# Performance work log

Hardware: AMD Instinct MI355X
Metric: run time of the kernel (lower is better)

The kernel has to match this reference:

```python
import jax, jax.numpy as jnp
import numpy as np

TAU = 0.07
EPS = 1e-6  # torch CosineSimilarity eps


def setup_inputs() -> dict:
    key = jax.random.key(0)
    k1, k2, k3 = jax.random.split(key, 3)
    n, d, n_classes = 8192, 256, 1024
    imitation_embeds = jax.random.normal(k1, (n, d), dtype=jnp.float32)
    recording_embeds = jax.random.normal(k2, (n, d), dtype=jnp.float32)
    labels = jax.random.randint(k3, (n,), 0, n_classes, dtype=jnp.int64)
    return {
        "imitation_embeds": imitation_embeds,
        "recording_embeds": recording_embeds,
        "labels": labels,
    }


def reference(imitation_embeds, recording_embeds, labels):
    n = imitation_embeds.shape[0]
    # cosine similarity with per-vector norm clamp (torch semantics)
    im_n = imitation_embeds / jnp.maximum(
        jnp.linalg.norm(imitation_embeds, axis=1, keepdims=True), EPS)
    rec_n = recording_embeds / jnp.maximum(
        jnp.linalg.norm(recording_embeds, axis=1, keepdims=True), EPS)
    i2r = jnp.einsum("nd,md->nm", im_n, rec_n) / TAU  # [n, n]

    same = labels[:, None] == labels[None, :]          # [n, n] bool
    eye = jnp.eye(n, dtype=bool)
    # original: mask = ~(same ^ diag_embed(diag(same))); diag(same) is all True
    # -> keep the diagonal (positive) and all different-label negatives
    mask = ~(same ^ eye)

    # per-row masked log-softmax evaluated at the diagonal entry:
    # log_softmax(row[mask])[pos_of_diag] = i2r[i,i] - logsumexp(row over mask)
    lse = jax.nn.logsumexp(jnp.where(mask, i2r, -jnp.inf), axis=1)  # [n]
    loss = -jnp.mean(jnp.diagonal(i2r) - lse)
    return loss
```

## Files before the change

kernel.cpp:

```cpp
#include <hip/hip_runtime.h>

#define N 8192
#define D 256
#define INV_TAU 14.285714285714286f
#define SCALE2 20.60992915555662f
#define EPSN 1e-6f
#define MAXM 48

#define RT 256
#define CT 64
#define CSPLIT 16
#define CPB (N / CSPLIT)
#define NTILES (CPB / CT)

typedef unsigned int u32x4 __attribute__((ext_vector_type(4)));
typedef __bf16 bf16x8 __attribute__((ext_vector_type(8)));
typedef float f32x4 __attribute__((ext_vector_type(4)));

__device__ inline unsigned short f2bf(float x) {
    unsigned int u = __builtin_bit_cast(unsigned int, x);
    u += 0x7fffu + ((u >> 16) & 1u);
    return (unsigned short)(u >> 16);
}
__device__ inline float b2f(unsigned short u) {
    unsigned int x = (unsigned int)u << 16;
    return __builtin_bit_cast(float, x);
}
__device__ inline float fexp2(float x) {
#if __has_builtin(__builtin_amdgcn_exp2f)
    return __builtin_amdgcn_exp2f(x);
#else
    return __expf(x * 0.6931471805599453f);
#endif
}

__global__ void ntx_prep(const float* __restrict__ im, const float* __restrict__ rec,
                         const int* __restrict__ labels,
                         unsigned short* __restrict__ A, unsigned short* __restrict__ Bm,
                         float* __restrict__ diag, float* __restrict__ rowsum,
                         int* __restrict__ cnt, unsigned short* __restrict__ members) {
    const int wave = threadIdx.x >> 6;
    const int lane = threadIdx.x & 63;
    const int row  = blockIdx.x * 4 + wave;

    const float4 a = ((const float4*)(im  + (size_t)row * D))[lane];
    const float4 b = ((const float4*)(rec + (size_t)row * D))[lane];

    float ssa = a.x*a.x + a.y*a.y + a.z*a.z + a.w*a.w;
    float ssb = b.x*b.x + b.y*b.y + b.z*b.z + b.w*b.w;
    float dt  = a.x*b.x + a.y*b.y + a.z*b.z + a.w*b.w;
    #pragma unroll
    for (int o = 32; o; o >>= 1) {
        ssa += __shfl_xor(ssa, o);
        ssb += __shfl_xor(ssb, o);
        dt  += __shfl_xor(dt , o);
    }
    const float ra = 1.0f / fmaxf(sqrtf(ssa), EPSN);
    const float rb = 1.0f / fmaxf(sqrtf(ssb), EPSN);

    ushort4 pa, pb;
    pa.x = f2bf(a.x*ra); pa.y = f2bf(a.y*ra); pa.z = f2bf(a.z*ra); pa.w = f2bf(a.w*ra);
    pb.x = f2bf(b.x*rb); pb.y = f2bf(b.y*rb); pb.z = f2bf(b.z*rb); pb.w = f2bf(b.w*rb);

    *(ushort4*)(A + (size_t)row * D + lane * 4) = pa;
    const int chunk = lane >> 1;
    const int sw = chunk ^ (row & 7);
    *(ushort4*)(Bm + (size_t)row * D + sw * 8 + (lane & 1) * 4) = pb;

    if (lane == 0) {
        diag[row]   = dt * ra * rb * INV_TAU;
        rowsum[row] = 0.0f;
        const int lab = labels[row];
        const int u = atomicAdd(&cnt[lab], 1);
        if (u < MAXM) members[lab * MAXM + u] = (unsigned short)row;
    }
}

__global__ __launch_bounds__(256, 2)
void ntx_lse(const unsigned short* __restrict__ A, const unsigned short* __restrict__ Bm,
             float* __restrict__ rowsum) {
    __shared__ __align__(16) unsigned short Bs[CT][D];

    const int wave = threadIdx.x >> 6;
    const int lane = threadIdx.x & 63;
    const int g    = lane >> 4;
    const int n16  = lane & 15;

    const int rowblk = blockIdx.x & (N / RT - 1);
    const int colblk = blockIdx.x >> 5;
    const int row0 = rowblk * RT + wave * 64;
    const int col0 = colblk * CPB;

    bf16x8 afrag[4][8];
    #pragma unroll
    for (int rs = 0; rs < 4; ++rs) {
        const int r = row0 + rs * 16 + n16;
        #pragma unroll
        for (int k = 0; k < 8; ++k)
            afrag[rs][k] = __builtin_bit_cast(
                bf16x8, *(const u32x4*)(A + (size_t)r * D + k * 32 + g * 8));
    }

    float acc[4][4];
    #pragma unroll
    for (int rs = 0; rs < 4; ++rs)
        #pragma unroll
        for (int q = 0; q < 4; ++q) acc[rs][q] = 0.f;

    for (int t = 0; t < NTILES; ++t) {
        const char* gsrc = (const char*)(Bm + (size_t)(col0 + t * CT) * D);
        char* lbase = (char*)&Bs[0][0];
        #pragma unroll
        for (int i = 0; i < 8; ++i) {
            const int off = (i * 4 + wave) * 1024;
            __builtin_amdgcn_global_load_lds(
                (const __attribute__((address_space(1))) void*)(gsrc + off + lane * 16),
                (__attribute__((address_space(3))) void*)(lbase + off),
                16, 0, 0);
        }
        __syncthreads();

        #pragma unroll
        for (int cs = 0; cs < 4; ++cs) {
            const int bc = cs * 16 + n16;
            bf16x8 bfrag[8];
            #pragma unroll
            for (int k = 0; k < 8; ++k)
                bfrag[k] = __builtin_bit_cast(
                    bf16x8, *(const u32x4*)(&Bs[bc][((k * 4 + g) ^ (bc & 7)) * 8]));

            #pragma unroll
            for (int rs = 0; rs < 4; ++rs) {
                f32x4 c = {0.f, 0.f, 0.f, 0.f};
                #pragma unroll
                for (int k = 0; k < 8; ++k)
                    c = __builtin_amdgcn_mfma_f32_16x16x32_bf16(
                            afrag[rs][k], bfrag[k], c, 0, 0, 0);
                #pragma unroll
                for (int q = 0; q < 4; ++q)
                    acc[rs][q] += fexp2(c[q] * SCALE2);
            }
        }
        __syncthreads();
    }

    #pragma unroll
    for (int rs = 0; rs < 4; ++rs)
        #pragma unroll
        for (int q = 0; q < 4; ++q) {
            float v = acc[rs][q];
            v += __shfl_xor(v, 1);
            v += __shfl_xor(v, 2);
            v += __shfl_xor(v, 4);
            v += __shfl_xor(v, 8);
            if (n16 == 0)
                atomicAdd(&rowsum[row0 + rs * 16 + g * 4 + q], v);
        }
}

__global__ void ntx_correct(const unsigned short* __restrict__ A,
                            const unsigned short* __restrict__ Bm,
                            const int* __restrict__ labels, const int* __restrict__ cnt,
                            const unsigned short* __restrict__ members,
                            float* __restrict__ rowsum) {
    const int wave = threadIdx.x >> 6;
    const int lane = threadIdx.x & 63;
    const int W = blockIdx.x * 4 + wave;
    const int chunk = lane >> 1;

    for (int rr = 0; rr < 4; ++rr) {
        const int r = W * 4 + rr;
        const int lab = labels[r];
        const int m = min(cnt[lab], MAXM);
        const ushort4 av = *(const ushort4*)(A + (size_t)r * D + lane * 4);
        const float a0 = b2f(av.x), a1 = b2f(av.y), a2 = b2f(av.z), a3 = b2f(av.w);
        float sum = 0.f;
        for (int t = 0; t < m; ++t) {
            const int j = members[lab * MAXM + t];
            if (j == r) continue;
            const int sw = chunk ^ (j & 7);
            const ushort4 bv = *(const ushort4*)(Bm + (size_t)j * D + sw * 8 + (lane & 1) * 4);
            float d = a0 * b2f(bv.x) + a1 * b2f(bv.y) + a2 * b2f(bv.z) + a3 * b2f(bv.w);
            #pragma unroll
            for (int o = 32; o; o >>= 1) d += __shfl_xor(d, o);
            sum += fexp2(d * SCALE2);
        }
        if (lane == 0) rowsum[r] -= sum;
    }
}

__global__ void ntx_finish(const float* __restrict__ diag,
                           const float* __restrict__ rowsum,
                           float* __restrict__ out) {
    __shared__ float red[256];
    float s = 0.f;
    for (int i = threadIdx.x; i < N; i += 256)
        s += logf(rowsum[i]) - diag[i];
    red[threadIdx.x] = s;
    __syncthreads();
    #pragma unroll
    for (int o = 128; o; o >>= 1) {
        if (threadIdx.x < o) red[threadIdx.x] += red[threadIdx.x + o];
        __syncthreads();
    }
    if (threadIdx.x == 0) out[0] = red[0] / (float)N;
}

extern "C" void kernel_launch(void* const* d_in, const int* in_sizes, int n_in,
                              void* d_out, int out_size, void* d_ws, size_t ws_size,
                              hipStream_t stream) {
    const float* im     = (const float*)d_in[0];
    const float* rec    = (const float*)d_in[1];
    const int*   labels = (const int*)d_in[2];
    float* out = (float*)d_out;

    unsigned short* A  = (unsigned short*)d_ws;
    unsigned short* Bm = A + (size_t)N * D;
    float* diag   = (float*)(Bm + (size_t)N * D);
    float* rowsum = diag + N;
    int* cnt      = (int*)(rowsum + N);
    unsigned short* members = (unsigned short*)(cnt + 1024);

    hipMemsetAsync(cnt, 0, 1024 * sizeof(int), stream);
    ntx_prep<<<N / 4, 256, 0, stream>>>(im, rec, labels, A, Bm, diag, rowsum, cnt, members);
    ntx_lse<<<(N / RT) * CSPLIT, 256, 0, stream>>>(A, Bm, rowsum);
    ntx_correct<<<N / 16, 256, 0, stream>>>(A, Bm, labels, cnt, members, rowsum);
    ntx_finish<<<1, 256, 0, stream>>>(diag, rowsum, out);
}
```

Baseline: 149.7 us.

## Double-buffer LDS tiles, fold exp scale into A, move log into correction kernel

The LSE kernel now double-buffers the B tile in LDS, prefetching the next tile before computing the current one and dropping one barrier per iteration. The SCALE2 factor is folded into the normalized A rows during prep, which removes a multiply per exponent in the inner loop. The correction kernel now uses one wave per row and computes the per-row log term, so the final reduction only sums precomputed values. The changes cost double the LDS footprint, which may affect occupancy, and add rounding risk because the scaled bf16 values are not unit vectors.

```diff
diff --git a/kernel.cpp b/kernel.cpp
--- a/kernel.cpp
+++ b/kernel.cpp
@@ -4,8 +4,9 @@
 #define D 256
 #define INV_TAU 14.285714285714286f
 #define SCALE2 20.60992915555662f
+#define LN2F 0.6931471805599453f
 #define EPSN 1e-6f
-#define MAXM 48
+#define MAXM 64
 
 #define RT 256
 #define CT 64
@@ -55,8 +56,8 @@
         ssb += __shfl_xor(ssb, o);
         dt  += __shfl_xor(dt , o);
     }
-    const float ra = 1.0f / fmaxf(sqrtf(ssa), EPSN);
-    const float rb = 1.0f / fmaxf(sqrtf(ssb), EPSN);
+    const float ra = SCALE2 / fmaxf(sqrtf(ssa), EPSN);
+    const float rb = 1.0f   / fmaxf(sqrtf(ssb), EPSN);
 
     ushort4 pa, pb;
     pa.x = f2bf(a.x*ra); pa.y = f2bf(a.y*ra); pa.z = f2bf(a.z*ra); pa.w = f2bf(a.w*ra);
@@ -68,7 +69,7 @@
     *(ushort4*)(Bm + (size_t)row * D + sw * 8 + (lane & 1) * 4) = pb;
 
     if (lane == 0) {
-        diag[row]   = dt * ra * rb * INV_TAU;
+        diag[row]   = (dt / SCALE2) * ra * rb * INV_TAU;
         rowsum[row] = 0.0f;
         const int lab = labels[row];
         const int u = atomicAdd(&cnt[lab], 1);
@@ -79,7 +80,7 @@
 __global__ __launch_bounds__(256, 2)
 void ntx_lse(const unsigned short* __restrict__ A, const unsigned short* __restrict__ Bm,
              float* __restrict__ rowsum) {
-    __shared__ __align__(16) unsigned short Bs[CT][D];
+    __shared__ __align__(16) unsigned short Bs[2][CT][D];
 
     const int wave = threadIdx.x >> 6;
     const int lane = threadIdx.x & 63;
@@ -107,18 +108,28 @@
         #pragma unroll
         for (int q = 0; q < 4; ++q) acc[rs][q] = 0.f;
 
+    const char* gbase = (const char*)(Bm + (size_t)col0 * D);
+
+    #define STAGE(t, buf)                                                          \
+        {                                                                          \
+            const char* gsrc = gbase + (t) * (CT * D * 2);                         \
+            char* lbase = (char*)&Bs[buf][0][0];                                   \
+            _Pragma("unroll")                                                      \
+            for (int i = 0; i < 8; ++i) {                                          \
+                const int off = (i * 4 + wave) * 1024;                             \
+                __builtin_amdgcn_global_load_lds(                                  \
+                    (const __attribute__((address_space(1))) void*)(gsrc + off + lane * 16), \
+                    (__attribute__((address_space(3))) void*)(lbase + off),        \
+                    16, 0, 0);                                                     \
+            }                                                                      \
+        }
+
+    STAGE(0, 0)
+
     for (int t = 0; t < NTILES; ++t) {
-        const char* gsrc = (const char*)(Bm + (size_t)(col0 + t * CT) * D);
-        char* lbase = (char*)&Bs[0][0];
-        #pragma unroll
-        for (int i = 0; i < 8; ++i) {
-            const int off = (i * 4 + wave) * 1024;
-            __builtin_amdgcn_global_load_lds(
-                (const __attribute__((address_space(1))) void*)(gsrc + off + lane * 16),
-                (__attribute__((address_space(3))) void*)(lbase + off),
-                16, 0, 0);
-        }
         __syncthreads();
+        if (t + 1 < NTILES) STAGE(t + 1, (t + 1) & 1)
+        const int buf = t & 1;
 
         #pragma unroll
         for (int cs = 0; cs < 4; ++cs) {
@@ -127,7 +138,7 @@
             #pragma unroll
             for (int k = 0; k < 8; ++k)
                 bfrag[k] = __builtin_bit_cast(
-                    bf16x8, *(const u32x4*)(&Bs[bc][((k * 4 + g) ^ (bc & 7)) * 8]));
+                    bf16x8, *(const u32x4*)(&Bs[buf][bc][((k * 4 + g) ^ (bc & 7)) * 8]));
 
             #pragma unroll
             for (int rs = 0; rs < 4; ++rs) {
@@ -138,10 +149,9 @@
                             afrag[rs][k], bfrag[k], c, 0, 0, 0);
                 #pragma unroll
                 for (int q = 0; q < 4; ++q)
-                    acc[rs][q] += fexp2(c[q] * SCALE2);
+                    acc[rs][q] += fexp2(c[q]);
             }
         }
-        __syncthreads();
     }
 
     #pragma unroll
@@ -158,44 +168,43 @@
         }
 }
 
-__global__ void ntx_correct(const unsigned short* __restrict__ A,
-                            const unsigned short* __restrict__ Bm,
-                            const int* __restrict__ labels, const int* __restrict__ cnt,
-                            const unsigned short* __restrict__ members,
-                            float* __restrict__ rowsum) {
+__global__ void ntx_corr(const unsigned short* __restrict__ A,
+                         const unsigned short* __restrict__ Bm,
+                         const int* __restrict__ labels, const int* __restrict__ cnt,
+                         const unsigned short* __restrict__ members,
+                         const float* __restrict__ diag,
+                         const float* __restrict__ rowsum,
+                         float* __restrict__ loss) {
     const int wave = threadIdx.x >> 6;
     const int lane = threadIdx.x & 63;
-    const int W = blockIdx.x * 4 + wave;
+    const int r = blockIdx.x * 4 + wave;
     const int chunk = lane >> 1;
 
-    for (int rr = 0; rr < 4; ++rr) {
-        const int r = W * 4 + rr;
-        const int lab = labels[r];
-        const int m = min(cnt[lab], MAXM);
-        const ushort4 av = *(const ushort4*)(A + (size_t)r * D + lane * 4);
-        const float a0 = b2f(av.x), a1 = b2f(av.y), a2 = b2f(av.z), a3 = b2f(av.w);
-        float sum = 0.f;
-        for (int t = 0; t < m; ++t) {
-            const int j = members[lab * MAXM + t];
-            if (j == r) continue;
-            const int sw = chunk ^ (j & 7);
-            const ushort4 bv = *(const ushort4*)(Bm + (size_t)j * D + sw * 8 + (lane & 1) * 4);
-            float d = a0 * b2f(bv.x) + a1 * b2f(bv.y) + a2 * b2f(bv.z) + a3 * b2f(bv.w);
-            #pragma unroll
-            for (int o = 32; o; o >>= 1) d += __shfl_xor(d, o);
-            sum += fexp2(d * SCALE2);
-        }
-        if (lane == 0) rowsum[r] -= sum;
-    }
-}
-
-__global__ void ntx_finish(const float* __restrict__ diag,
-                           const float* __restrict__ rowsum,
-                           float* __restrict__ out) {
+    const int lab = labels[r];
+    const int m = min(cnt[lab], MAXM);
+
+    const ushort4 av = *(const ushort4*)(A + (size_t)r * D + lane * 4);
+    const float a0 = b2f(av.x), a1 = b2f(av.y), a2 = b2f(av.z), a3 = b2f(av.w);
+
+    float sum = 0.f;
+    for (int t = 0; t < m; ++t) {
+        const int j = members[lab * MAXM + t];
+        if (j == r) continue;
+        const int sw = chunk ^ (j & 7);
+        const ushort4 bv = *(const ushort4*)(Bm + (size_t)j * D + sw * 8 + (lane & 1) * 4);
+        float d = a0 * b2f(bv.x) + a1 * b2f(bv.y) + a2 * b2f(bv.z) + a3 * b2f(bv.w);
+        #pragma unroll
+        for (int o = 32; o; o >>= 1) d += __shfl_xor(d, o);
+        sum += fexp2(d);
+    }
+    if (lane == 0)
+        loss[r] = log2f(rowsum[r] - sum) * LN2F - diag[r];
+}
+
+__global__ void ntx_final(const float* __restrict__ loss, float* __restrict__ out) {
     __shared__ float red[256];
     float s = 0.f;
-    for (int i = threadIdx.x; i < N; i += 256)
-        s += logf(rowsum[i]) - diag[i];
+    for (int i = threadIdx.x; i < N; i += 256) s += loss[i];
     red[threadIdx.x] = s;
     __syncthreads();
     #pragma unroll
@@ -218,12 +227,13 @@
     unsigned short* Bm = A + (size_t)N * D;
     float* diag   = (float*)(Bm + (size_t)N * D);
     float* rowsum = diag + N;
-    int* cnt      = (int*)(rowsum + N);
+    float* loss   = rowsum + N;
+    int* cnt      = (int*)(loss + N);
     unsigned short* members = (unsigned short*)(cnt + 1024);
 
     hipMemsetAsync(cnt, 0, 1024 * sizeof(int), stream);
     ntx_prep<<<N / 4, 256, 0, stream>>>(im, rec, labels, A, Bm, diag, rowsum, cnt, members);
     ntx_lse<<<(N / RT) * CSPLIT, 256, 0, stream>>>(A, Bm, rowsum);
-    ntx_correct<<<N / 16, 256, 0, stream>>>(A, Bm, labels, cnt, members, rowsum);
-    ntx_finish<<<1, 256, 0, stream>>>(diag, rowsum, out);
-}
+    ntx_corr<<<N / 4, 256, 0, stream>>>(A, Bm, labels, cnt, members, diag, rowsum, loss);
+    ntx_final<<<1, 256, 0, stream>>>(loss, out);
+}
```

Result: faster. 127.8 us (-14.6%).

## Shrink LSE row tile, double column split, fold scale into A, fuse finish

Applied to the files above, without the earlier changes.

Halves the per-wave row tile in the LSE kernel and doubles the column split, raising launch-bounds occupancy to 4 blocks. Folds the exp2 scale factor into the normalized A rows so the inner loop skips a multiply. Merges the final reduction into the correction kernel with a per-block atomicAdd, removing one launch. The smaller tile halves B-fragment reuse per wave, adding LDS traffic per MFMA, and the scaling before bf16 rounding slightly changes numerics.

```diff
diff --git a/kernel.cpp b/kernel.cpp
--- a/kernel.cpp
+++ b/kernel.cpp
@@ -4,12 +4,13 @@
 #define D 256
 #define INV_TAU 14.285714285714286f
 #define SCALE2 20.60992915555662f
+#define LN2F 0.6931471805599453f
 #define EPSN 1e-6f
-#define MAXM 48
-
-#define RT 256
+#define MAXM 64
+
+#define RT 128
 #define CT 64
-#define CSPLIT 16
+#define CSPLIT 32
 #define CPB (N / CSPLIT)
 #define NTILES (CPB / CT)
 
@@ -38,7 +39,8 @@
                          const int* __restrict__ labels,
                          unsigned short* __restrict__ A, unsigned short* __restrict__ Bm,
                          float* __restrict__ diag, float* __restrict__ rowsum,
-                         int* __restrict__ cnt, unsigned short* __restrict__ members) {
+                         int* __restrict__ cnt, unsigned short* __restrict__ members,
+                         float* __restrict__ out) {
     const int wave = threadIdx.x >> 6;
     const int lane = threadIdx.x & 63;
     const int row  = blockIdx.x * 4 + wave;
@@ -55,8 +57,8 @@
         ssb += __shfl_xor(ssb, o);
         dt  += __shfl_xor(dt , o);
     }
-    const float ra = 1.0f / fmaxf(sqrtf(ssa), EPSN);
-    const float rb = 1.0f / fmaxf(sqrtf(ssb), EPSN);
+    const float ra = SCALE2 / fmaxf(sqrtf(ssa), EPSN);
+    const float rb = 1.0f   / fmaxf(sqrtf(ssb), EPSN);
 
     ushort4 pa, pb;
     pa.x = f2bf(a.x*ra); pa.y = f2bf(a.y*ra); pa.z = f2bf(a.z*ra); pa.w = f2bf(a.w*ra);
@@ -68,15 +70,16 @@
     *(ushort4*)(Bm + (size_t)row * D + sw * 8 + (lane & 1) * 4) = pb;
 
     if (lane == 0) {
-        diag[row]   = dt * ra * rb * INV_TAU;
+        diag[row]   = (dt / SCALE2) * ra * rb * INV_TAU;
         rowsum[row] = 0.0f;
         const int lab = labels[row];
         const int u = atomicAdd(&cnt[lab], 1);
         if (u < MAXM) members[lab * MAXM + u] = (unsigned short)row;
-    }
-}
-
-__global__ __launch_bounds__(256, 2)
+        if (row == 0) out[0] = 0.0f;
+    }
+}
+
+__global__ __launch_bounds__(256, 4)
 void ntx_lse(const unsigned short* __restrict__ A, const unsigned short* __restrict__ Bm,
              float* __restrict__ rowsum) {
     __shared__ __align__(16) unsigned short Bs[CT][D];
@@ -87,13 +90,13 @@
     const int n16  = lane & 15;
 
     const int rowblk = blockIdx.x & (N / RT - 1);
-    const int colblk = blockIdx.x >> 5;
-    const int row0 = rowblk * RT + wave * 64;
+    const int colblk = blockIdx.x >> 6;
+    const int row0 = rowblk * RT + wave * 32;
     const int col0 = colblk * CPB;
 
-    bf16x8 afrag[4][8];
+    bf16x8 afrag[2][8];
     #pragma unroll
-    for (int rs = 0; rs < 4; ++rs) {
+    for (int rs = 0; rs < 2; ++rs) {
         const int r = row0 + rs * 16 + n16;
         #pragma unroll
         for (int k = 0; k < 8; ++k)
@@ -101,22 +104,22 @@
                 bf16x8, *(const u32x4*)(A + (size_t)r * D + k * 32 + g * 8));
     }
 
-    float acc[4][4];
-    #pragma unroll
-    for (int rs = 0; rs < 4; ++rs)
-        #pragma unroll
-        for (int q = 0; q < 4; ++q) acc[rs][q] = 0.f;
+    float acc[2][4] = {{0.f,0.f,0.f,0.f},{0.f,0.f,0.f,0.f}};
+
+    const char* gbase = (const char*)(Bm + (size_t)col0 * D);
 
     for (int t = 0; t < NTILES; ++t) {
-        const char* gsrc = (const char*)(Bm + (size_t)(col0 + t * CT) * D);
-        char* lbase = (char*)&Bs[0][0];
-        #pragma unroll
-        for (int i = 0; i < 8; ++i) {
-            const int off = (i * 4 + wave) * 1024;
-            __builtin_amdgcn_global_load_lds(
-                (const __attribute__((address_space(1))) void*)(gsrc + off + lane * 16),
-                (__attribute__((address_space(3))) void*)(lbase + off),
-                16, 0, 0);
+        {
+            const char* gsrc = gbase + t * (CT * D * 2);
+            char* lbase = (char*)&Bs[0][0];
+            #pragma unroll
+            for (int i = 0; i < 8; ++i) {
+                const int off = (i * 4 + wave) * 1024;
+                __builtin_amdgcn_global_load_lds(
+                    (const __attribute__((address_space(1))) void*)(gsrc + off + lane * 16),
+                    (__attribute__((address_space(3))) void*)(lbase + off),
+                    16, 0, 0);
+            }
         }
         __syncthreads();
 
@@ -130,7 +133,7 @@
                     bf16x8, *(const u32x4*)(&Bs[bc][((k * 4 + g) ^ (bc & 7)) * 8]));
 
             #pragma unroll
-            for (int rs = 0; rs < 4; ++rs) {
+            for (int rs = 0; rs < 2; ++rs) {
                 f32x4 c = {0.f, 0.f, 0.f, 0.f};
                 #pragma unroll
                 for (int k = 0; k < 8; ++k)
@@ -138,14 +141,14 @@
                             afrag[rs][k], bfrag[k], c, 0, 0, 0);
                 #pragma unroll
                 for (int q = 0; q < 4; ++q)
-                    acc[rs][q] += fexp2(c[q] * SCALE2);
+                    acc[rs][q] += fexp2(c[q]);
             }
         }
         __syncthreads();
     }
 
     #pragma unroll
-    for (int rs = 0; rs < 4; ++rs)
+    for (int rs = 0; rs < 2; ++rs)
         #pragma unroll
         for (int q = 0; q < 4; ++q) {
             float v = acc[rs][q];
@@ -158,22 +161,28 @@
         }
 }
 
-__global__ void ntx_correct(const unsigned short* __restrict__ A,
-                            const unsigned short* __restrict__ Bm,
-                            const int* __restrict__ labels, const int* __restrict__ cnt,
-                            const unsigned short* __restrict__ members,
-                            float* __restrict__ rowsum) {
+__global__ void ntx_corr(const unsigned short* __restrict__ A,
+                         const unsigned short* __restrict__ Bm,
+                         const int* __restrict__ labels, const int* __restrict__ cnt,
+                         const unsigned short* __restrict__ members,
+                         const float* __restrict__ diag,
+                         const float* __restrict__ rowsum,
+                         float* __restrict__ out) {
+    __shared__ float wred[4];
     const int wave = threadIdx.x >> 6;
     const int lane = threadIdx.x & 63;
-    const int W = blockIdx.x * 4 + wave;
+    const int w = blockIdx.x * 4 + wave;
     const int chunk = lane >> 1;
 
+    float lsum = 0.f;
     for (int rr = 0; rr < 4; ++rr) {
-        const int r = W * 4 + rr;
+        const int r = w * 4 + rr;
         const int lab = labels[r];
         const int m = min(cnt[lab], MAXM);
+
         const ushort4 av = *(const ushort4*)(A + (size_t)r * D + lane * 4);
         const float a0 = b2f(av.x), a1 = b2f(av.y), a2 = b2f(av.z), a3 = b2f(av.w);
+
         float sum = 0.f;
         for (int t = 0; t < m; ++t) {
             const int j = members[lab * MAXM + t];
@@ -183,27 +192,14 @@
             float d = a0 * b2f(bv.x) + a1 * b2f(bv.y) + a2 * b2f(bv.z) + a3 * b2f(bv.w);
             #pragma unroll
             for (int o = 32; o; o >>= 1) d += __shfl_xor(d, o);
-            sum += fexp2(d * SCALE2);
-        }
-        if (lane == 0) rowsum[r] -= sum;
-    }
-}
-
-__global__ void ntx_finish(const float* __restrict__ diag,
-                           const float* __restrict__ rowsum,
-                           float* __restrict__ out) {
-    __shared__ float red[256];
-    float s = 0.f;
-    for (int i = threadIdx.x; i < N; i += 256)
-        s += logf(rowsum[i]) - diag[i];
-    red[threadIdx.x] = s;
+            sum += fexp2(d);
+        }
+        lsum += log2f(rowsum[r] - sum) * LN2F - diag[r];
+    }
+    if (lane == 0) wred[wave] = lsum;
     __syncthreads();
-    #pragma unroll
-    for (int o = 128; o; o >>= 1) {
-        if (threadIdx.x < o) red[threadIdx.x] += red[threadIdx.x + o];
-        __syncthreads();
-    }
-    if (threadIdx.x == 0) out[0] = red[0] / (float)N;
+    if (threadIdx.x == 0)
+        atomicAdd(out, (wred[0] + wred[1] + wred[2] + wred[3]) * (1.0f / (float)N));
 }
 
 extern "C" void kernel_launch(void* const* d_in, const int* in_sizes, int n_in,
@@ -222,8 +218,7 @@
     unsigned short* members = (unsigned short*)(cnt + 1024);
 
     hipMemsetAsync(cnt, 0, 1024 * sizeof(int), stream);
-    ntx_prep<<<N / 4, 256, 0, stream>>>(im, rec, labels, A, Bm, diag, rowsum, cnt, members);
+    ntx_prep<<<N / 4, 256, 0, stream>>>(im, rec, labels, A, Bm, diag, rowsum, cnt, members, out);
     ntx_lse<<<(N / RT) * CSPLIT, 256, 0, stream>>>(A, Bm, rowsum);
-    ntx_correct<<<N / 16, 256, 0, stream>>>(A, Bm, labels, cnt, members, rowsum);
-    ntx_finish<<<1, 256, 0, stream>>>(diag, rowsum, out);
-}
+    ntx_corr<<<N / 16, 256, 0, stream>>>(A, Bm, labels, cnt, members, diag, rowsum, out);
+}
```

New measurement: 153.3 us. 1.02x slower.
